# Kernel optimization log

Hardware: AMD Instinct MI355X
Metric: run time of the kernel (lower is better)

The kernel has to match this reference:

```python
import jax, jax.numpy as jnp
import numpy as np

N, CIN, H, W = 4, 64, 160, 256
INS_PER = 16
T = N * INS_PER            # total instances = sum(num_ins)
CH, OUT = 16, 1
WN = [(CIN + 2) * CH, CH * CH, CH * OUT]   # [1056, 256, 16]
BN = [CH, CH, OUT]
P = sum(WN) + sum(BN)      # 1361
MASK_BIAS_SHIFT = 2.19


def setup_inputs() -> dict:
    key = jax.random.key(0)
    k1, k2 = jax.random.split(key)
    x = jax.random.normal(k1, (N, CIN, H, W), dtype=jnp.float32)
    mask_head_params = jax.random.normal(k2, (T, P), dtype=jnp.float32) * 0.1
    num_ins = jnp.full((N,), INS_PER, dtype=jnp.int32)
    return {"x": x, "mask_head_params": mask_head_params, "num_ins": num_ins}


def reference(x, mask_head_params, num_ins):
    n, c, h, w = x.shape
    # compute_locations with stride=1: locations = stack((shift_x, shift_y)) + 0
    # NOTE: the original `locations[:0] /= H` / `locations[:1] /= W` are
    # zero-size slices (no-ops), so coords remain unnormalized.
    ys, xs = jnp.meshgrid(jnp.arange(h, dtype=jnp.float32),
                          jnp.arange(w, dtype=jnp.float32), indexing='ij')
    loc = jnp.stack([xs, ys], axis=0)                       # [2, H, W]
    loc = jnp.broadcast_to(loc[None], (n, 2, h, w))
    xc = jnp.concatenate([loc, x], axis=1)                  # [N, C+2, H, W]

    # per-image repeat -> one feature copy per instance
    feat = jnp.repeat(xc, num_ins, axis=0, total_repeat_length=T)  # [T, C+2, H, W]

    # parse dynamic params (mask=True: last bias shifted by -2.19)
    p = mask_head_params
    o = 0
    w0 = p[:, o:o + WN[0]].reshape(T, CH, CIN + 2); o += WN[0]
    w1 = p[:, o:o + WN[1]].reshape(T, CH, CH);      o += WN[1]
    w2 = p[:, o:o + WN[2]].reshape(T, OUT, CH);     o += WN[2]
    b0 = p[:, o:o + BN[0]]; o += BN[0]
    b1 = p[:, o:o + BN[1]]; o += BN[1]
    b2 = p[:, o:o + BN[2]] - MASK_BIAS_SHIFT

    # grouped 1x1 convs (groups=num_insts) == per-instance linear over HxW
    hdn = jax.nn.relu(jnp.einsum('toi,tihw->tohw', w0, feat) + b0[:, :, None, None])
    hdn = jax.nn.relu(jnp.einsum('toi,tihw->tohw', w1, hdn) + b1[:, :, None, None])
    out = jnp.einsum('toi,tihw->tohw', w2, hdn) + b2[:, :, None, None]
    return out.reshape(1, T * OUT, h, w)
```

## Files before the change

### kernel.cpp

```cpp
#include <hip/hip_runtime.h>


#define CIN  64
#define HH   160
#define WW   256
#define HWSZ (HH * WW)
#define PP   1361
#define MASK_BIAS_SHIFT 2.19f
#define PKF  1344
#define NSPLIT 2

typedef short short8 __attribute__((ext_vector_type(8)));
typedef float f32x4  __attribute__((ext_vector_type(4)));

union BF8 { short8 s; __bf16 b[8]; };

__device__ inline __bf16 bhi(float v) { return (__bf16)v; }
__device__ inline __bf16 blo(float v) { return (__bf16)(v - (float)(__bf16)v); }


__global__ __launch_bounds__(64) void prep_params(
    const float* __restrict__ params, float* __restrict__ pk)
{
    const int t    = blockIdx.x;
    const int lane = threadIdx.x;
    const int col  = lane & 15;
    const int g    = lane >> 4;
    const float* pw = params + (size_t)t * PP;
    float* dst = pk + (size_t)t * PKF;

    const __bf16 z = (__bf16)0.f;

    BF8 a00, a01;
#pragma unroll
    for (int j = 0; j < 8; ++j) {
        a00.b[j] = (__bf16)pw[col * 66 + 2 +      g * 8 + j];
        a01.b[j] = (__bf16)pw[col * 66 + 2 + 32 + g * 8 + j];
    }

    BF8 a1b;
#pragma unroll
    for (int j = 0; j < 4; ++j)
        a1b.b[j] = (__bf16)pw[1056 + col * 16 + g * 4 + j];
    {
        const float b1 = pw[1344 + col];
        a1b.b[4] = (g == 0) ? bhi(b1) : z;
        a1b.b[5] = (g == 0) ? blo(b1) : z;
        a1b.b[6] = z;  a1b.b[7] = z;
    }

    BF8 a2r;
#pragma unroll
    for (int j = 0; j < 4; ++j) a2r.b[j] = (__bf16)pw[1312 + g * 4 + j];
    a2r.b[4] = z; a2r.b[5] = z; a2r.b[6] = z; a2r.b[7] = z;

    BF8 ca;
    {
        const float wx = pw[col * 66 + 0];
        const float wy = pw[col * 66 + 1];
        const float b0 = pw[1328 + col];
        ca.b[0] = (g == 0) ? bhi(wx) : z;
        ca.b[1] = (g == 0) ? blo(wx) : z;
        ca.b[2] = (g == 0) ? bhi(wy) : z;
        ca.b[3] = (g == 0) ? blo(wy) : z;
        ca.b[4] = (g == 0) ? bhi(b0) : z;
        ca.b[5] = (g == 0) ? blo(b0) : z;
        ca.b[6] = z; ca.b[7] = z;
    }

    ((short8*)(dst       ))[lane] = a00.s;
    ((short8*)(dst +  256))[lane] = a01.s;
    ((short8*)(dst +  512))[lane] = a1b.s;
    ((short8*)(dst +  768))[lane] = a2r.s;
    ((short8*)(dst + 1024))[lane] = ca.s;
    if (lane == 0) dst[1280] = pw[1360] - MASK_BIAS_SHIFT;
}

__global__ __launch_bounds__(256, 4) void mask_head_v5(
    const float* __restrict__ x,
    const float* __restrict__ pk,
    const int*   __restrict__ num_ins,
    float*       __restrict__ out,
    int N, int T)
{
    const int tid  = threadIdx.x;
    const int wave = tid >> 6;
    const int lane = tid & 63;
    const int col  = lane & 15;
    const int g    = lane >> 4;
    const int n    = blockIdx.y;
    const int s    = blockIdx.z;
    const int pxw  = blockIdx.x * 256 + wave * 64;

    int t0 = 0;
    for (int j = 0; j < n; ++j) t0 += num_ins[j];
    int t1 = t0 + num_ins[n];
    if (n == N - 1) t1 = T;
    if (t1 > T) t1 = T;
    t0 = __builtin_amdgcn_readfirstlane(t0);
    t1 = __builtin_amdgcn_readfirstlane(t1);

    BF8 xb[4][2];
    const float* xbase = x + (size_t)n * CIN * HWSZ + pxw + col;
#pragma unroll
    for (int nt = 0; nt < 4; ++nt)
#pragma unroll
        for (int c = 0; c < 2; ++c)
#pragma unroll
            for (int j = 0; j < 8; ++j) {
                const int ch = c * 32 + g * 8 + j;
                xb[nt][c].b[j] = (__bf16)xbase[(size_t)ch * HWSZ + nt * 16];
            }

    BF8 b2c[4];
#pragma unroll
    for (int nt = 0; nt < 4; ++nt) {
        const int px = pxw + nt * 16 + col;
        const __bf16 xfb = (__bf16)(float)(px & (WW - 1));
        const __bf16 yfb = (__bf16)(float)(px >> 8);
        b2c[nt].b[0] = xfb; b2c[nt].b[1] = xfb;
        b2c[nt].b[2] = yfb; b2c[nt].b[3] = yfb;
        b2c[nt].b[4] = (__bf16)1.f; b2c[nt].b[5] = (__bf16)1.f;
        b2c[nt].b[6] = (__bf16)0.f; b2c[nt].b[7] = (__bf16)0.f;
    }

    const __bf16 one = (__bf16)1.f, zero = (__bf16)0.f;

    for (int t = t0 + s; t < t1; t += NSPLIT) {
        const float* pt = pk + (size_t)t * PKF;

        short8 a00 = ((const short8*)(pt       ))[lane];
        short8 a01 = ((const short8*)(pt +  256))[lane];
        short8 a1b = ((const short8*)(pt +  512))[lane];
        short8 a2r = ((const short8*)(pt +  768))[lane];
        short8 ca  = ((const short8*)(pt + 1024))[lane];
        const float b2v = pt[1280];

        float oval = 0.f;
#pragma unroll
        for (int nt = 0; nt < 4; ++nt) {
            f32x4 acc0 = {0.f, 0.f, 0.f, 0.f};
            acc0 = __builtin_amdgcn_mfma_f32_16x16x32_bf16(ca,  b2c[nt].s,  acc0, 0, 0, 0);
            acc0 = __builtin_amdgcn_mfma_f32_16x16x32_bf16(a00, xb[nt][0].s, acc0, 0, 0, 0);
            acc0 = __builtin_amdgcn_mfma_f32_16x16x32_bf16(a01, xb[nt][1].s, acc0, 0, 0, 0);

            BF8 h0;
#pragma unroll
            for (int j = 0; j < 4; ++j) h0.b[j] = (__bf16)fmaxf(acc0[j], 0.f);
            h0.b[4] = one; h0.b[5] = one; h0.b[6] = zero; h0.b[7] = zero;

            f32x4 acc1 = {0.f, 0.f, 0.f, 0.f};
            acc1 = __builtin_amdgcn_mfma_f32_16x16x32_bf16(a1b, h0.s, acc1, 0, 0, 0);

            BF8 h1;
#pragma unroll
            for (int j = 0; j < 4; ++j) h1.b[j] = (__bf16)fmaxf(acc1[j], 0.f);
            h1.b[4] = zero; h1.b[5] = zero; h1.b[6] = zero; h1.b[7] = zero;

            f32x4 acc2 = {0.f, 0.f, 0.f, 0.f};
            acc2 = __builtin_amdgcn_mfma_f32_16x16x32_bf16(a2r, h1.s, acc2, 0, 0, 0);

            if (nt == g) oval = acc2[0] + b2v;
        }
        out[(size_t)t * HWSZ + pxw + lane] = oval;
    }
}

__global__ __launch_bounds__(256) void mask_head_mfma_nows(
    const float* __restrict__ x,
    const float* __restrict__ params,
    const int*   __restrict__ num_ins,
    float*       __restrict__ out,
    int N, int T)
{
    const int tid  = threadIdx.x;
    const int wave = tid >> 6;
    const int lane = tid & 63;
    const int col  = lane & 15;
    const int g    = lane >> 4;
    const int n    = blockIdx.y;
    const int pxw  = blockIdx.x * 256 + wave * 64;

    int t0 = 0;
    for (int j = 0; j < n; ++j) t0 += num_ins[j];
    int t1 = t0 + num_ins[n];
    if (n == N - 1) t1 = T;
    if (t1 > T) t1 = T;

    BF8 xb[4][2];
    const float* xbase = x + (size_t)n * CIN * HWSZ + pxw + col;
#pragma unroll
    for (int nt = 0; nt < 4; ++nt)
#pragma unroll
        for (int c = 0; c < 2; ++c)
#pragma unroll
            for (int j = 0; j < 8; ++j)
                xb[nt][c].b[j] = (__bf16)xbase[(size_t)(c * 32 + g * 8 + j) * HWSZ + nt * 16];

    float xf[4], yf[4];
#pragma unroll
    for (int nt = 0; nt < 4; ++nt) {
        const int pix = pxw + nt * 16 + col;
        xf[nt] = (float)(pix & (WW - 1));
        yf[nt] = (float)(pix >> 8);
    }

    for (int t = t0; t < t1; ++t) {
        const float* pw = params + (size_t)t * PP;
        BF8 a00, a01, a1;
#pragma unroll
        for (int j = 0; j < 8; ++j) {
            a00.b[j] = (__bf16)pw[col * 66 + 2 +      g * 8 + j];
            a01.b[j] = (__bf16)pw[col * 66 + 2 + 32 + g * 8 + j];
        }
#pragma unroll
        for (int j = 0; j < 4; ++j) {
            a1.b[j]     = (__bf16)pw[1056 + col * 16 + g * 4 + j];
            a1.b[4 + j] = (__bf16)0.f;
        }
        float wxv[4], wyv[4], b0v[4], b1v[4], w2v[4];
#pragma unroll
        for (int j = 0; j < 4; ++j) {
            const int r = g * 4 + j;
            wxv[j] = pw[r * 66 + 0];
            wyv[j] = pw[r * 66 + 1];
            b0v[j] = pw[1328 + r];
            b1v[j] = pw[1344 + r];
            w2v[j] = pw[1312 + r];
        }
        const float b2v = pw[1360] - MASK_BIAS_SHIFT;

        f32x4 acc0[4];
#pragma unroll
        for (int nt = 0; nt < 4; ++nt) {
            f32x4 a = {0.f, 0.f, 0.f, 0.f};
            a = __builtin_amdgcn_mfma_f32_16x16x32_bf16(a00.s, xb[nt][0].s, a, 0, 0, 0);
            a = __builtin_amdgcn_mfma_f32_16x16x32_bf16(a01.s, xb[nt][1].s, a, 0, 0, 0);
            acc0[nt] = a;
        }
        BF8 h0[4];
#pragma unroll
        for (int nt = 0; nt < 4; ++nt)
#pragma unroll
            for (int j = 0; j < 4; ++j) {
                float v = acc0[nt][j] + b0v[j];
                v = fmaf(wxv[j], xf[nt], v);
                v = fmaf(wyv[j], yf[nt], v);
                v = fmaxf(v, 0.f);
                h0[nt].b[j]     = (__bf16)v;
                h0[nt].b[4 + j] = (__bf16)0.f;
            }
        f32x4 acc1[4];
#pragma unroll
        for (int nt = 0; nt < 4; ++nt) {
            f32x4 a = {0.f, 0.f, 0.f, 0.f};
            acc1[nt] = __builtin_amdgcn_mfma_f32_16x16x32_bf16(a1.s, h0[nt].s, a, 0, 0, 0);
        }
        float oval = 0.f;
#pragma unroll
        for (int nt = 0; nt < 4; ++nt) {
            float sum = 0.f;
#pragma unroll
            for (int j = 0; j < 4; ++j) {
                const float h = fmaxf(acc1[nt][j] + b1v[j], 0.f);
                sum = fmaf(w2v[j], h, sum);
            }
            sum += __shfl_xor(sum, 16, 64);
            sum += __shfl_xor(sum, 32, 64);
            if (nt == g) oval = sum + b2v;
        }
        out[(size_t)t * HWSZ + pxw + lane] = oval;
    }
}

extern "C" void kernel_launch(void* const* d_in, const int* in_sizes, int n_in,
                              void* d_out, int out_size, void* d_ws, size_t ws_size,
                              hipStream_t stream) {
    const float* x      = (const float*)d_in[0];
    const float* params = (const float*)d_in[1];
    const int*   nins   = (const int*)d_in[2];
    float*       out    = (float*)d_out;

    const int N = in_sizes[2];
    const int T = in_sizes[1] / PP;
    const size_t ws_needed = (size_t)T * PKF * sizeof(float);

    if (ws_size >= ws_needed) {
        float* pk = (float*)d_ws;
        prep_params<<<T, dim3(64), 0, stream>>>(params, pk);
        dim3 grid(HWSZ / 256, N, NSPLIT);
        mask_head_v5<<<grid, dim3(256), 0, stream>>>(x, pk, nins, out, N, T);
    } else {
        dim3 grid(HWSZ / 256, N);
        mask_head_mfma_nows<<<grid, dim3(256), 0, stream>>>(x, params, nins, out, N, T);
    }
}
```

Baseline: 31.17 us.

## Assign one 16-pixel tile per wave and loop all instances per block

Each wave now owns a single 16-pixel tile instead of four, and the grid grows fourfold in the pixel dimension. The instance split across blockIdx.z is removed, so each block walks every instance of its image. Output stores are batched over groups of four instances so each lane group writes one instance row, and occupancy is raised to 8 blocks per CU. This cuts register pressure and the redundant per-instance MFMA work, at the cost of reloading the per-instance parameters for every 16-pixel tile.

```diff
diff --git a/kernel.cpp b/kernel.cpp
--- a/kernel.cpp
+++ b/kernel.cpp
@@ -8,7 +8,6 @@
 #define PP   1361
 #define MASK_BIAS_SHIFT 2.19f
 #define PKF  1344
-#define NSPLIT 2
 
 typedef short short8 __attribute__((ext_vector_type(8)));
 typedef float f32x4  __attribute__((ext_vector_type(4)));
@@ -76,7 +75,7 @@
     if (lane == 0) dst[1280] = pw[1360] - MASK_BIAS_SHIFT;
 }
 
-__global__ __launch_bounds__(256, 4) void mask_head_v5(
+__global__ __launch_bounds__(256, 8) void mask_head_v6(
     const float* __restrict__ x,
     const float* __restrict__ pk,
     const int*   __restrict__ num_ins,
@@ -89,8 +88,7 @@
     const int col  = lane & 15;
     const int g    = lane >> 4;
     const int n    = blockIdx.y;
-    const int s    = blockIdx.z;
-    const int pxw  = blockIdx.x * 256 + wave * 64;
+    const int pxt  = blockIdx.x * 64 + wave * 16;
 
     int t0 = 0;
     for (int j = 0; j < n; ++j) t0 += num_ins[j];
@@ -99,34 +97,34 @@
     if (t1 > T) t1 = T;
     t0 = __builtin_amdgcn_readfirstlane(t0);
     t1 = __builtin_amdgcn_readfirstlane(t1);
-
-    BF8 xb[4][2];
-    const float* xbase = x + (size_t)n * CIN * HWSZ + pxw + col;
-#pragma unroll
-    for (int nt = 0; nt < 4; ++nt)
-#pragma unroll
-        for (int c = 0; c < 2; ++c)
-#pragma unroll
-            for (int j = 0; j < 8; ++j) {
-                const int ch = c * 32 + g * 8 + j;
-                xb[nt][c].b[j] = (__bf16)xbase[(size_t)ch * HWSZ + nt * 16];
-            }
-
-    BF8 b2c[4];
-#pragma unroll
-    for (int nt = 0; nt < 4; ++nt) {
-        const int px = pxw + nt * 16 + col;
+    const int M = t1 - t0;
+
+    BF8 xb0, xb1;
+    const float* xbase = x + (size_t)n * CIN * HWSZ + pxt + col;
+#pragma unroll
+    for (int j = 0; j < 8; ++j) {
+        xb0.b[j] = (__bf16)xbase[(size_t)(     g * 8 + j) * HWSZ];
+        xb1.b[j] = (__bf16)xbase[(size_t)(32 + g * 8 + j) * HWSZ];
+    }
+
+    BF8 b2c;
+    {
+        const int px = pxt + col;
         const __bf16 xfb = (__bf16)(float)(px & (WW - 1));
         const __bf16 yfb = (__bf16)(float)(px >> 8);
-        b2c[nt].b[0] = xfb; b2c[nt].b[1] = xfb;
-        b2c[nt].b[2] = yfb; b2c[nt].b[3] = yfb;
-        b2c[nt].b[4] = (__bf16)1.f; b2c[nt].b[5] = (__bf16)1.f;
-        b2c[nt].b[6] = (__bf16)0.f; b2c[nt].b[7] = (__bf16)0.f;
+        b2c.b[0] = xfb; b2c.b[1] = xfb;
+        b2c.b[2] = yfb; b2c.b[3] = yfb;
+        b2c.b[4] = (__bf16)1.f; b2c.b[5] = (__bf16)1.f;
+        b2c.b[6] = (__bf16)0.f; b2c.b[7] = (__bf16)0.f;
     }
 
     const __bf16 one = (__bf16)1.f, zero = (__bf16)0.f;
-
-    for (int t = t0 + s; t < t1; t += NSPLIT) {
+    float* const obase = out + pxt + col;
+
+    float oval = 0.f;
+#pragma unroll 4
+    for (int m = 0; m < M; ++m) {
+        const int t = t0 + m;
         const float* pt = pk + (size_t)t * PKF;
 
         short8 a00 = ((const short8*)(pt       ))[lane];
@@ -136,34 +134,35 @@
         short8 ca  = ((const short8*)(pt + 1024))[lane];
         const float b2v = pt[1280];
 
-        float oval = 0.f;
-#pragma unroll
-        for (int nt = 0; nt < 4; ++nt) {
-            f32x4 acc0 = {0.f, 0.f, 0.f, 0.f};
-            acc0 = __builtin_amdgcn_mfma_f32_16x16x32_bf16(ca,  b2c[nt].s,  acc0, 0, 0, 0);
-            acc0 = __builtin_amdgcn_mfma_f32_16x16x32_bf16(a00, xb[nt][0].s, acc0, 0, 0, 0);
-            acc0 = __builtin_amdgcn_mfma_f32_16x16x32_bf16(a01, xb[nt][1].s, acc0, 0, 0, 0);
-
-            BF8 h0;
-#pragma unroll
-            for (int j = 0; j < 4; ++j) h0.b[j] = (__bf16)fmaxf(acc0[j], 0.f);
-            h0.b[4] = one; h0.b[5] = one; h0.b[6] = zero; h0.b[7] = zero;
-
-            f32x4 acc1 = {0.f, 0.f, 0.f, 0.f};
-            acc1 = __builtin_amdgcn_mfma_f32_16x16x32_bf16(a1b, h0.s, acc1, 0, 0, 0);
-
-            BF8 h1;
-#pragma unroll
-            for (int j = 0; j < 4; ++j) h1.b[j] = (__bf16)fmaxf(acc1[j], 0.f);
-            h1.b[4] = zero; h1.b[5] = zero; h1.b[6] = zero; h1.b[7] = zero;
-
-            f32x4 acc2 = {0.f, 0.f, 0.f, 0.f};
-            acc2 = __builtin_amdgcn_mfma_f32_16x16x32_bf16(a2r, h1.s, acc2, 0, 0, 0);
-
-            if (nt == g) oval = acc2[0] + b2v;
-        }
-        out[(size_t)t * HWSZ + pxw + lane] = oval;
-    }
+        f32x4 acc0 = {0.f, 0.f, 0.f, 0.f};
+        acc0 = __builtin_amdgcn_mfma_f32_16x16x32_bf16(ca,  b2c.s, acc0, 0, 0, 0);
+        acc0 = __builtin_amdgcn_mfma_f32_16x16x32_bf16(a00, xb0.s, acc0, 0, 0, 0);
+        acc0 = __builtin_amdgcn_mfma_f32_16x16x32_bf16(a01, xb1.s, acc0, 0, 0, 0);
+
+        BF8 h0;
+#pragma unroll
+        for (int j = 0; j < 4; ++j) h0.b[j] = (__bf16)fmaxf(acc0[j], 0.f);
+        h0.b[4] = one; h0.b[5] = one; h0.b[6] = zero; h0.b[7] = zero;
+
+        f32x4 acc1 = {0.f, 0.f, 0.f, 0.f};
+        acc1 = __builtin_amdgcn_mfma_f32_16x16x32_bf16(a1b, h0.s, acc1, 0, 0, 0);
+
+        BF8 h1;
+#pragma unroll
+        for (int j = 0; j < 4; ++j) h1.b[j] = (__bf16)fmaxf(acc1[j], 0.f);
+        h1.b[4] = zero; h1.b[5] = zero; h1.b[6] = zero; h1.b[7] = zero;
+
+        f32x4 acc2 = {0.f, 0.f, 0.f, 0.f};
+        acc2 = __builtin_amdgcn_mfma_f32_16x16x32_bf16(a2r, h1.s, acc2, 0, 0, 0);
+
+        const float res = acc2[0] + b2v;
+        if ((m & 3) == g) oval = res;
+        if ((m & 3) == 3)
+            obase[(size_t)(t - 3 + g) * HWSZ] = oval;
+    }
+    const int rem = M & 3;
+    if (rem && g < rem)
+        obase[(size_t)(t1 - rem + g) * HWSZ] = oval;
 }
 
 __global__ __launch_bounds__(256) void mask_head_mfma_nows(
@@ -288,8 +287,8 @@
     if (ws_size >= ws_needed) {
         float* pk = (float*)d_ws;
         prep_params<<<T, dim3(64), 0, stream>>>(params, pk);
-        dim3 grid(HWSZ / 256, N, NSPLIT);
-        mask_head_v5<<<grid, dim3(256), 0, stream>>>(x, pk, nins, out, N, T);
+        dim3 grid(HWSZ / 64, N, 1);
+        mask_head_v6<<<grid, dim3(256), 0, stream>>>(x, pk, nins, out, N, T);
     } else {
         dim3 grid(HWSZ / 256, N);
         mask_head_mfma_nows<<<grid, dim3(256), 0, stream>>>(x, params, nins, out, N, T);
```

Result: slower. 42.05 us (+34.9%).

## Stage per-instance params in double-buffered LDS and drop instance split

Applied to the files above, without the earlier changes.

Each block now loops over every instance of its image instead of splitting instances across two z-blocks. The packed parameters for each instance are loaded once per block into shared memory, replacing a global load by every wave. The next instance's parameters are prefetched into registers and written to the other LDS buffer, overlapping the fetch with the MFMA work. This halves the grid and reloads of x features but adds a __syncthreads per instance and reduces parallelism per image.

```diff
diff --git a/kernel.cpp b/kernel.cpp
--- a/kernel.cpp
+++ b/kernel.cpp
@@ -8,7 +8,6 @@
 #define PP   1361
 #define MASK_BIAS_SHIFT 2.19f
 #define PKF  1344
-#define NSPLIT 2
 
 typedef short short8 __attribute__((ext_vector_type(8)));
 typedef float f32x4  __attribute__((ext_vector_type(4)));
@@ -76,20 +75,21 @@
     if (lane == 0) dst[1280] = pw[1360] - MASK_BIAS_SHIFT;
 }
 
-__global__ __launch_bounds__(256, 4) void mask_head_v5(
+__global__ __launch_bounds__(256, 4) void mask_head_v7(
     const float* __restrict__ x,
     const float* __restrict__ pk,
     const int*   __restrict__ num_ins,
     float*       __restrict__ out,
     int N, int T)
 {
+    __shared__ __align__(16) float plds[2][PKF];
+
     const int tid  = threadIdx.x;
     const int wave = tid >> 6;
     const int lane = tid & 63;
     const int col  = lane & 15;
     const int g    = lane >> 4;
     const int n    = blockIdx.y;
-    const int s    = blockIdx.z;
     const int pxw  = blockIdx.x * 256 + wave * 64;
 
     int t0 = 0;
@@ -99,6 +99,8 @@
     if (t1 > T) t1 = T;
     t0 = __builtin_amdgcn_readfirstlane(t0);
     t1 = __builtin_amdgcn_readfirstlane(t1);
+    const int M = t1 - t0;
+    if (M <= 0) return;
 
     BF8 xb[4][2];
     const float* xbase = x + (size_t)n * CIN * HWSZ + pxw + col;
@@ -126,21 +128,39 @@
 
     const __bf16 one = (__bf16)1.f, zero = (__bf16)0.f;
 
-    for (int t = t0 + s; t < t1; t += NSPLIT) {
-        const float* pt = pk + (size_t)t * PKF;
-
-        short8 a00 = ((const short8*)(pt       ))[lane];
-        short8 a01 = ((const short8*)(pt +  256))[lane];
-        short8 a1b = ((const short8*)(pt +  512))[lane];
-        short8 a2r = ((const short8*)(pt +  768))[lane];
-        short8 ca  = ((const short8*)(pt + 1024))[lane];
-        const float b2v = pt[1280];
+    {
+        const f32x4* src = (const f32x4*)(pk + (size_t)t0 * PKF);
+        f32x4* dst = (f32x4*)plds[0];
+        dst[tid] = src[tid];
+        if (tid < 80) dst[256 + tid] = src[256 + tid];
+    }
+    __syncthreads();
+
+    int cur = 0;
+    for (int m = 0; m < M; ++m) {
+        const int t = t0 + m;
+
+        const bool have_next = (m + 1 < M);
+        f32x4 s0, s1;
+        if (have_next) {
+            const f32x4* src = (const f32x4*)(pk + (size_t)(t + 1) * PKF);
+            s0 = src[tid];
+            if (tid < 80) s1 = src[256 + tid];
+        }
+
+        const short8* fp = (const short8*)plds[cur];
+        short8 a00 = fp[lane];
+        short8 a01 = fp[ 64 + lane];
+        short8 a1b = fp[128 + lane];
+        short8 a2r = fp[192 + lane];
+        short8 ca  = fp[256 + lane];
+        const float b2v = plds[cur][1280];
 
         float oval = 0.f;
 #pragma unroll
         for (int nt = 0; nt < 4; ++nt) {
             f32x4 acc0 = {0.f, 0.f, 0.f, 0.f};
-            acc0 = __builtin_amdgcn_mfma_f32_16x16x32_bf16(ca,  b2c[nt].s,  acc0, 0, 0, 0);
+            acc0 = __builtin_amdgcn_mfma_f32_16x16x32_bf16(ca,  b2c[nt].s,   acc0, 0, 0, 0);
             acc0 = __builtin_amdgcn_mfma_f32_16x16x32_bf16(a00, xb[nt][0].s, acc0, 0, 0, 0);
             acc0 = __builtin_amdgcn_mfma_f32_16x16x32_bf16(a01, xb[nt][1].s, acc0, 0, 0, 0);
 
@@ -163,6 +183,14 @@
             if (nt == g) oval = acc2[0] + b2v;
         }
         out[(size_t)t * HWSZ + pxw + lane] = oval;
+
+        if (have_next) {
+            f32x4* dst = (f32x4*)plds[cur ^ 1];
+            dst[tid] = s0;
+            if (tid < 80) dst[256 + tid] = s1;
+        }
+        __syncthreads();
+        cur ^= 1;
     }
 }
 
@@ -288,8 +316,8 @@
     if (ws_size >= ws_needed) {
         float* pk = (float*)d_ws;
         prep_params<<<T, dim3(64), 0, stream>>>(params, pk);
-        dim3 grid(HWSZ / 256, N, NSPLIT);
-        mask_head_v5<<<grid, dim3(256), 0, stream>>>(x, pk, nins, out, N, T);
+        dim3 grid(HWSZ / 256, N);
+        mask_head_v7<<<grid, dim3(256), 0, stream>>>(x, pk, nins, out, N, T);
     } else {
         dim3 grid(HWSZ / 256, N);
         mask_head_mfma_nows<<<grid, dim3(256), 0, stream>>>(x, params, nins, out, N, T);
```

Result: slower. 32.67 us (+4.8%).
